# Performance work log

Hardware: AMD Instinct MI355X
Metric: run time of the kernel (lower is better)

The kernel has to match this reference:

```python
import jax, jax.numpy as jnp
import numpy as np

REG = 1.0
LAM1 = REG * 0.1
LAM2 = REG * 0.15
TAU = 0.01
RHO = 1.99
SIGMA = 1.0 / TAU / 72.0


def epsilon(I):
    # I: (c,h,w,2) -> G: (c,h,w,4); symmetrized gradient stencil
    I0, I1 = I[..., 0], I[..., 1]
    g0 = I0 - jnp.pad(I0[:, :-1, :], ((0, 0), (1, 0), (0, 0)))
    g1 = jnp.pad(I0[:, :, 1:] - I0[:, :, :-1], ((0, 0), (0, 0), (1, 0)))
    g2 = I1 - jnp.pad(I1[:, :, :-1], ((0, 0), (0, 0), (1, 0)))
    g3 = jnp.pad(I1[:, 1:, :] - I1[:, :-1, :], ((0, 0), (0, 1), (0, 0)))
    return jnp.stack([g0, g1, g2, g3], axis=-1)


def epsilonT(G):
    # G: (c,h,w,4) -> I: (c,h,w,2); adjoint of epsilon
    g0, g1, g2, g3 = G[..., 0], G[..., 1], G[..., 2], G[..., 3]
    i0 = g0 - jnp.pad(g0[:, 1:, :], ((0, 0), (0, 1), (0, 0)))
    A = g1[:, :, 1:]
    i0 = i0 + jnp.pad(A, ((0, 0), (0, 0), (1, 0))) - jnp.pad(A, ((0, 0), (0, 0), (0, 1)))
    i1 = g2 - jnp.pad(g2[:, :, 1:], ((0, 0), (0, 0), (0, 1)))
    B = g3[:, :-1, :]
    i1 = i1 + jnp.pad(B, ((0, 0), (1, 0), (0, 0))) - jnp.pad(B, ((0, 0), (0, 1), (0, 0)))
    return jnp.stack([i0, i1], axis=-1)


def nabla(I):
    # I: (c,h,w) -> G: (c,h,w,2); forward differences, zero at far boundary
    g0 = jnp.pad(I[:, 1:, :] - I[:, :-1, :], ((0, 0), (0, 1), (0, 0)))
    g1 = jnp.pad(I[:, :, 1:] - I[:, :, :-1], ((0, 0), (0, 0), (0, 1)))
    return jnp.stack([g0, g1], axis=-1)


def nablaT(G):
    # G: (c,h,w,2) -> I: (c,h,w); negative divergence (adjoint of nabla)
    A = G[:, :-1, :, 0]
    B = G[:, :, :-1, 1]
    return (jnp.pad(A, ((0, 0), (1, 0), (0, 0))) - jnp.pad(A, ((0, 0), (0, 1), (0, 0)))
            + jnp.pad(B, ((0, 0), (0, 0), (1, 0))) - jnp.pad(B, ((0, 0), (0, 0), (0, 1))))


def prox_tau_fx(x, y):
    return (x + TAU * y) / (1.0 + TAU)


def prox_tau_fr(r):
    left = jnp.sqrt(jnp.sum(r ** 2, axis=3)) / (TAU * LAM1)
    return r - r / jnp.maximum(left, 1.0)[..., None]


def prox_sigma_g_conj(u):
    return u / jnp.maximum(jnp.sqrt(jnp.sum(u ** 2, axis=3)) / LAM2, 1.0)[..., None]


def setup_inputs() -> dict:
    key = jax.random.key(0)
    y = jax.random.normal(key, (3, 512, 512), dtype=jnp.float32)
    return {"y": y, "n_it_max": 30}


def reference(y, n_it_max):
    c, h, w = y.shape
    x2 = y
    r2 = jnp.zeros((c, h, w, 2), dtype=y.dtype)
    u2 = jnp.zeros((c, h, w, 4), dtype=y.dtype)

    def step(carry, _):
        x2, r2, u2 = carry
        tmp = TAU * epsilonT(u2)
        x = prox_tau_fx(x2 - nablaT(tmp), y)
        r = prox_tau_fr(r2 + tmp)
        u = prox_sigma_g_conj(u2 + SIGMA * epsilon(nabla(2.0 * x - x2) - (2.0 * r - r2)))
        x2 = x2 + RHO * (x - x2)
        r2 = r2 + RHO * (r - r2)
        u2 = u2 + RHO * (u - u2)
        return (x2, r2, u2), None

    (x2, r2, u2), _ = jax.lax.scan(step, (x2, r2, u2), None, length=n_it_max)
    return (x2, r2, u2)
```

## Files before the change

kernel.cpp:

```cpp
#include <hip/hip_runtime.h>
#include <type_traits>


#define H 512
#define W 512
#define C 3
#define HW (H * W)
#define CHW (C * H * W)
#define N_IT 30

#define TW 64
#define TH 8

#define TAU     0.01f
#define LAM2    0.15f
#define RHO     1.99f
#define SIGMA   1.3888888888888888f
#define TL1     0.001f
#define INV_1PT (1.0f / 1.01f)

#define BROWS 10
#define BSTR  72

typedef _Float16 f16;
typedef __attribute__((ext_vector_type(4))) _Float16 h4;
typedef __attribute__((ext_vector_type(8))) _Float16 h8;


template <int MODE>
__global__ __launch_bounds__(192)
void fused_it(const float* __restrict__ y,
              const float* __restrict__ srcX,
              const f16*   __restrict__ srcH,
              float*       __restrict__ dstX,
              f16*         __restrict__ dstH,
              float*       __restrict__ outp)
{
    __shared__ float sb[3][BROWS][BSTR];

    const int tid = threadIdx.x;
    const int c   = blockIdx.z;
    const int i0  = blockIdx.y * TH;
    const int j0  = blockIdx.x * TW;
    const int cb  = c * HW;

    const bool edge = (MODE == 0) ||
                      (blockIdx.x == 0) || (blockIdx.x == W / TW - 1) ||
                      (blockIdx.y == 0) || (blockIdx.y == H / TH - 1);

    const f16* rSrc = srcH;
    const f16* uSrc = srcH + 2 * CHW;
    f16* rDst = dstH;
    f16* uDst = dstH ? dstH + 2 * CHW : nullptr;

    float cu0[4], cu1[4], cu2[4], cu3[4];

    auto strip1 = [&](auto SAFE_c, int rr, int s, bool interior) {
        constexpr bool SAFE = decltype(SAFE_c)::value;
        const int gi  = i0 + rr;
        const int gjb = j0 + s;
        const int p   = cb + gi * W + gjb;

        const bool rowC  = SAFE || ((unsigned)gi < H);
        const bool cMain = SAFE || ((unsigned)gjb < W);
        const bool okC   = rowC && cMain;

        float yv[4], x2c[4], r0c[4], r1c[4];
        if (okC) {
            *(float4*)yv = *(const float4*)(y + p);
        } else {
            yv[0] = yv[1] = yv[2] = yv[3] = 0.f;
        }
        if (MODE != 0) {
            if (okC) {
                *(float4*)x2c = *(const float4*)(srcX + p);
                const h8 rv = *(const h8*)(rSrc + 2 * p);
                #pragma unroll
                for (int e = 0; e < 4; ++e) {
                    r0c[e] = (float)rv[2 * e];
                    r1c[e] = (float)rv[2 * e + 1];
                }
            } else {
                #pragma unroll
                for (int e = 0; e < 4; ++e) { x2c[e] = 0.f; r0c[e] = 0.f; r1c[e] = 0.f; }
            }
        }

        float t0c[4], t1c[4], t0n[4], t1w[4];
        if (MODE == 0) {
            #pragma unroll
            for (int e = 0; e < 4; ++e) {
                x2c[e] = yv[e]; r0c[e] = 0.f; r1c[e] = 0.f;
                t0c[e] = t1c[e] = t0n[e] = t1w[e] = 0.f;
            }
            if (interior) {
                #pragma unroll
                for (int e = 0; e < 4; ++e) { cu0[e] = cu1[e] = cu2[e] = cu3[e] = 0.f; }
            }
        } else {
            const bool rowN = SAFE || ((unsigned)(gi - 1) < H);
            const bool rowS = SAFE || ((unsigned)(gi + 1) < H);
            const bool cm1  = SAFE || ((unsigned)(gjb - 1) < W);
            const bool c4   = SAFE || ((unsigned)(gjb + 4) < W);
            const int pN = p - W, pS = p + W;

            auto L4 = [&](int pp, bool ok) -> h4 {
                h4 z = {}; if (ok) z = *(const h4*)(uSrc + 4 * pp); return z;
            };
            auto L8 = [&](int pp, bool ok) -> h8 {
                h8 z = {}; if (ok) z = *(const h8*)(uSrc + 4 * pp); return z;
            };
            const h4 nA = L4(pN - 1, rowN && cm1);
            const h8 nB = L8(pN,     rowN && cMain);
            const h8 nC = L8(pN + 2, rowN && cMain);
            const h4 nD = L4(pN + 4, rowN && c4);
            const h4 cA = L4(p - 1,  rowC && cm1);
            const h8 cB = L8(p,      okC);
            const h8 cC = L8(p + 2,  okC);
            const h4 cD = L4(p + 4,  rowC && c4);
            const h8 sB = L8(pS,     rowS && cMain);
            const h8 sC = L8(pS + 2, rowS && cMain);

            const float u0c[4] = {(float)cB[0], (float)cB[4], (float)cC[0], (float)cC[4]};
            const float u1c[5] = {(float)cB[1], (float)cB[5], (float)cC[1], (float)cC[5], (float)cD[1]};
            const float u2r[6] = {(float)cA[2], (float)cB[2], (float)cB[6], (float)cC[2], (float)cC[6], (float)cD[2]};
            const float u3c[5] = {(float)cA[3], (float)cB[3], (float)cB[7], (float)cC[3], (float)cC[7]};
            const float u0n[4] = {(float)nB[0], (float)nB[4], (float)nC[0], (float)nC[4]};
            const float u1n[5] = {(float)nB[1], (float)nB[5], (float)nC[1], (float)nC[5], (float)nD[1]};
            const float u3n[5] = {(float)nA[3], (float)nB[3], (float)nB[7], (float)nC[3], (float)nC[7]};
            const float u0s[4] = {(float)sB[0], (float)sB[4], (float)sC[0], (float)sC[4]};

            if constexpr (SAFE) {
                #pragma unroll
                for (int e = 0; e < 4; ++e) {
                    t0c[e] = TAU * (u0c[e] - u0s[e] + u1c[e] - u1c[e + 1]);
                    t1c[e] = TAU * (u2r[e + 1] - u2r[e + 2] + u3n[e + 1] - u3c[e + 1]);
                    t0n[e] = TAU * (u0n[e] - u0c[e] + u1n[e] - u1n[e + 1]);
                    t1w[e] = TAU * (u2r[e] - u2r[e + 1] + u3n[e] - u3c[e]);
                }
            } else {
                const bool im0 = gi > 0, imHl = gi < H - 1;
                #pragma unroll
                for (int e = 0; e < 4; ++e) {
                    const int gj = gjb + e;
                    const bool jm0 = gj > 0;
                    t0c[e] = TAU * (u0c[e] - u0s[e] + (jm0 ? u1c[e] : 0.f) - u1c[e + 1]);
                    t1c[e] = TAU * (u2r[e + 1] - u2r[e + 2] + u3n[e + 1] - (imHl ? u3c[e + 1] : 0.f));
                    t0n[e] = im0 ? TAU * (u0n[e] - u0c[e] + (jm0 ? u1n[e] : 0.f) - u1n[e + 1]) : 0.f;
                    t1w[e] = jm0 ? TAU * (u2r[e] - u2r[e + 1] + u3n[e] - (imHl ? u3c[e] : 0.f)) : 0.f;
                }
            }
            if (interior) {
                #pragma unroll
                for (int e = 0; e < 4; ++e) {
                    cu0[e] = u0c[e]; cu1[e] = u1c[e];
                    cu2[e] = u2r[e + 1]; cu3[e] = u3c[e + 1];
                }
            }
        }

        float xnew[4], rn0[4], rn1[4], xb[4], rb0[4], rb1[4];
        {
            const bool imH = SAFE ? true : (gi < H - 1);
            #pragma unroll
            for (int e = 0; e < 4; ++e) {
                const int gj = gjb + e;
                const bool jmW = SAFE ? true : (gj < W - 1);
                const float nT  = t0n[e] - (imH ? t0c[e] : 0.f) + t1w[e] - (jmW ? t1c[e] : 0.f);
                const float xv  = (x2c[e] - nT + TAU * yv[e]) * INV_1PT;
                xb[e] = 2.f * xv - x2c[e];
                const float rp0 = r0c[e] + t0c[e];
                const float rp1 = r1c[e] + t1c[e];
                const float ss  = rp0 * rp0 + rp1 * rp1;
                const float f   = 1.f - fminf(TL1 * rsqrtf(ss), 1.f);
                const float rv0 = rp0 * f, rv1 = rp1 * f;
                rb0[e]  = 2.f * rv0 - r0c[e];
                rb1[e]  = 2.f * rv1 - r1c[e];
                xnew[e] = x2c[e] + RHO * (xv - x2c[e]);
                rn0[e]  = r0c[e] + RHO * (rv0 - r0c[e]);
                rn1[e]  = r1c[e] + RHO * (rv1 - r1c[e]);
            }
        }
        *(float4*)&sb[0][rr + 1][s + 4] = *(float4*)xb;
        *(float4*)&sb[1][rr + 1][s + 4] = *(float4*)rb0;
        *(float4*)&sb[2][rr + 1][s + 4] = *(float4*)rb1;

        if (interior) {
            if (MODE == 2) {
                *(float4*)(outp + p) = *(float4*)xnew;
                *(float4*)(outp + CHW + 2 * p)     = make_float4(rn0[0], rn1[0], rn0[1], rn1[1]);
                *(float4*)(outp + CHW + 2 * p + 4) = make_float4(rn0[2], rn1[2], rn0[3], rn1[3]);
            } else {
                *(float4*)(dstX + p) = *(float4*)xnew;
                h8 hr;
                #pragma unroll
                for (int e = 0; e < 4; ++e) {
                    hr[2 * e]     = (f16)rn0[e];
                    hr[2 * e + 1] = (f16)rn1[e];
                }
                *(h8*)(rDst + 2 * p) = hr;
            }
        }
    };

    auto ringmap = [&](int t, int& rr, int& s) {
        if (t < 18)      { rr = -1;      s = 4 * t - 4; }
        else if (t < 36) { rr = TH;      s = 4 * (t - 18) - 4; }
        else if (t < 44) { rr = t - 36;  s = -4; }
        else             { rr = t - 44;  s = TW; }
    };

    if (!edge) {
        if (tid < 128) {
            strip1(std::true_type{}, tid >> 4, 4 * (tid & 15), true);
        } else if (tid < 180) {
            int rr, s; ringmap(tid - 128, rr, s);
            strip1(std::true_type{}, rr, s, false);
        }
    } else {
        if (tid < 128) {
            strip1(std::false_type{}, tid >> 4, 4 * (tid & 15), true);
        } else if (tid < 180) {
            int rr, s; ringmap(tid - 128, rr, s);
            strip1(std::false_type{}, rr, s, false);
        }
    }
    __syncthreads();

    auto stage2 = [&](auto SAFE_c) {
        constexpr bool SAFE = decltype(SAFE_c)::value;
        const int tx = tid & 15, ty = tid >> 4;
        const int gi  = i0 + ty;
        const int gjb = j0 + 4 * tx;
        const int lr  = ty + 1;
        const int lc  = 4 * tx + 4;
        float4 v;
        float xA[6], xS[6], xN[4], r0C[5], r0N[4], r1C[5], r1S[4];
        xA[0] = sb[0][lr][lc - 1];
        v = *(const float4*)&sb[0][lr][lc]; xA[1]=v.x; xA[2]=v.y; xA[3]=v.z; xA[4]=v.w;
        xA[5] = sb[0][lr][lc + 4];
        xS[0] = sb[0][lr + 1][lc - 1];
        v = *(const float4*)&sb[0][lr + 1][lc]; xS[1]=v.x; xS[2]=v.y; xS[3]=v.z; xS[4]=v.w;
        xS[5] = sb[0][lr + 1][lc + 4];
        v = *(const float4*)&sb[0][lr - 1][lc]; xN[0]=v.x; xN[1]=v.y; xN[2]=v.z; xN[3]=v.w;
        r0C[0] = sb[1][lr][lc - 1];
        v = *(const float4*)&sb[1][lr][lc]; r0C[1]=v.x; r0C[2]=v.y; r0C[3]=v.z; r0C[4]=v.w;
        v = *(const float4*)&sb[1][lr - 1][lc]; r0N[0]=v.x; r0N[1]=v.y; r0N[2]=v.z; r0N[3]=v.w;
        r1C[0] = sb[2][lr][lc - 1];
        v = *(const float4*)&sb[2][lr][lc]; r1C[1]=v.x; r1C[2]=v.y; r1C[3]=v.z; r1C[4]=v.w;
        v = *(const float4*)&sb[2][lr + 1][lc]; r1S[0]=v.x; r1S[1]=v.y; r1S[2]=v.z; r1S[3]=v.w;

        const bool im0 = SAFE ? true : (gi > 0);
        const bool imH = SAFE ? true : (gi < H - 1);
        float un0[4], un1[4], un2[4], un3[4];
        #pragma unroll
        for (int e = 0; e < 4; ++e) {
            const int gj = gjb + e;
            const bool jm0 = SAFE ? true : (gj > 0);
            const bool jmW = SAFE ? true : (gj < W - 1);
            const float xC = xA[e + 1], xE = xA[e + 2], xW_ = xA[e];
            const float I0c = (imH ? xS[e + 1] - xC : 0.f) - r0C[e + 1];
            const float I0n = im0 ? (xC - xN[e] - r0N[e]) : 0.f;
            const float I0w = jm0 ? ((imH ? xS[e] - xW_ : 0.f) - r0C[e]) : 0.f;
            const float I1c = (jmW ? xE - xC : 0.f) - r1C[e + 1];
            const float I1w = jm0 ? (xC - xW_ - r1C[e]) : 0.f;
            const float I1s = imH ? ((jmW ? xS[e + 2] - xS[e + 1] : 0.f) - r1S[e]) : 0.f;
            const float g0 = I0c - I0n;
            const float g1 = jm0 ? (I0c - I0w) : 0.f;
            const float g2 = I1c - I1w;
            const float g3 = imH ? (I1s - I1c) : 0.f;
            const float up0 = cu0[e] + SIGMA * g0;
            const float up1 = cu1[e] + SIGMA * g1;
            const float up2 = cu2[e] + SIGMA * g2;
            const float up3 = cu3[e] + SIGMA * g3;
            const float ss  = up0 * up0 + up1 * up1 + up2 * up2 + up3 * up3;
            const float inv = fminf(LAM2 * rsqrtf(ss), 1.f);
            un0[e] = cu0[e] + RHO * (up0 * inv - cu0[e]);
            un1[e] = cu1[e] + RHO * (up1 * inv - cu1[e]);
            un2[e] = cu2[e] + RHO * (up2 * inv - cu2[e]);
            un3[e] = cu3[e] + RHO * (up3 * inv - cu3[e]);
        }
        const int p = cb + gi * W + gjb;
        if (MODE == 2) {
            #pragma unroll
            for (int e = 0; e < 4; ++e)
                *(float4*)(outp + 3 * CHW + 4 * (p + e)) =
                    make_float4(un0[e], un1[e], un2[e], un3[e]);
        } else {
            h8 w0, w1;
            #pragma unroll
            for (int e = 0; e < 2; ++e) {
                w0[4 * e + 0] = (f16)un0[e]; w0[4 * e + 1] = (f16)un1[e];
                w0[4 * e + 2] = (f16)un2[e]; w0[4 * e + 3] = (f16)un3[e];
            }
            #pragma unroll
            for (int e = 2; e < 4; ++e) {
                w1[4 * (e - 2) + 0] = (f16)un0[e]; w1[4 * (e - 2) + 1] = (f16)un1[e];
                w1[4 * (e - 2) + 2] = (f16)un2[e]; w1[4 * (e - 2) + 3] = (f16)un3[e];
            }
            *(h8*)(uDst + 4 * p)     = w0;
            *(h8*)(uDst + 4 * p + 8) = w1;
        }
    };

    if (tid < 128) {
        if (!edge) stage2(std::true_type{});
        else       stage2(std::false_type{});
    }
}

extern "C" void kernel_launch(void* const* d_in, const int* in_sizes, int n_in,
                              void* d_out, int out_size, void* d_ws, size_t ws_size,
                              hipStream_t stream) {
    const float* y = (const float*)d_in[0];
    float* out = (float*)d_out;

    float* x0 = (float*)d_ws;
    float* x1 = x0 + CHW;
    f16*   h0 = (f16*)(x1 + CHW);
    f16*   h1 = h0 + 6 * CHW;

    dim3 blk(192, 1, 1);
    dim3 grd(W / TW, H / TH, C);

    fused_it<0><<<grd, blk, 0, stream>>>(y, nullptr, nullptr, x0, h0, nullptr);
    for (int k = 2; k < N_IT; ++k) {
        const bool even = (k % 2 == 0);
        float* sx = even ? x0 : x1;  f16* sh = even ? h0 : h1;
        float* dx = even ? x1 : x0;  f16* dh = even ? h1 : h0;
        fused_it<1><<<grd, blk, 0, stream>>>(y, sx, sh, dx, dh, nullptr);
    }
    fused_it<2><<<grd, blk, 0, stream>>>(y, x0, h0, nullptr, nullptr, out);
}
```

Measured before the change: 335.2 us.

## Double tile height and process two rows per thread with shared vertical neighbors

Tile height doubles from 8 to 16 rows, and each of the 128 worker threads now computes two vertically adjacent rows in both stages. Loads of the u neighbor rows and shared-memory reads are reused between the two rows. This shrinks the redundant halo work and global loads per output. The cost is higher register pressure per thread and half as many blocks, which lowers parallelism.

```diff
diff --git a/kernel.cpp b/kernel.cpp
--- a/kernel.cpp
+++ b/kernel.cpp
@@ -10,7 +10,7 @@
 #define N_IT 30
 
 #define TW 64
-#define TH 8
+#define TH 16
 
 #define TAU     0.01f
 #define LAM2    0.15f
@@ -19,7 +19,7 @@
 #define TL1     0.001f
 #define INV_1PT (1.0f / 1.01f)
 
-#define BROWS 10
+#define BROWS 18
 #define BSTR  72
 
 typedef _Float16 f16;
@@ -53,16 +53,166 @@
     f16* rDst = dstH;
     f16* uDst = dstH ? dstH + 2 * CHW : nullptr;
 
-    float cu0[4], cu1[4], cu2[4], cu3[4];
-
-    auto strip1 = [&](auto SAFE_c, int rr, int s, bool interior) {
+    float cu0A[4], cu1A[4], cu2A[4], cu3A[4];
+    float cu0B[4], cu1B[4], cu2B[4], cu3B[4];
+
+    auto s1finish = [&](auto SAFE_c, int gi, int gjb, int p, int lrow, bool interior,
+                        const float* yv, const float* x2c, const float* r0c, const float* r1c,
+                        const float* t0c, const float* t1c, const float* t0n, const float* t1w) {
         constexpr bool SAFE = decltype(SAFE_c)::value;
+        const int s4 = gjb - j0 + 4;
+        const bool imH = SAFE ? true : (gi < H - 1);
+        float xb[4], rb0[4], rb1[4], xnew[4], rn0[4], rn1[4];
+        #pragma unroll
+        for (int e = 0; e < 4; ++e) {
+            const int gj = gjb + e;
+            const bool jmW = SAFE ? true : (gj < W - 1);
+            const float nT  = t0n[e] - (imH ? t0c[e] : 0.f) + t1w[e] - (jmW ? t1c[e] : 0.f);
+            const float xv  = (x2c[e] - nT + TAU * yv[e]) * INV_1PT;
+            xb[e] = 2.f * xv - x2c[e];
+            const float rp0 = r0c[e] + t0c[e];
+            const float rp1 = r1c[e] + t1c[e];
+            const float ss  = rp0 * rp0 + rp1 * rp1;
+            const float f   = 1.f - fminf(TL1 * rsqrtf(ss), 1.f);
+            const float rv0 = rp0 * f, rv1 = rp1 * f;
+            rb0[e]  = 2.f * rv0 - r0c[e];
+            rb1[e]  = 2.f * rv1 - r1c[e];
+            xnew[e] = x2c[e] + RHO * (xv - x2c[e]);
+            rn0[e]  = r0c[e] + RHO * (rv0 - r0c[e]);
+            rn1[e]  = r1c[e] + RHO * (rv1 - r1c[e]);
+        }
+        *(float4*)&sb[0][lrow][s4] = *(float4*)xb;
+        *(float4*)&sb[1][lrow][s4] = *(float4*)rb0;
+        *(float4*)&sb[2][lrow][s4] = *(float4*)rb1;
+
+        if (interior) {
+            if (MODE == 2) {
+                *(float4*)(outp + p) = *(float4*)xnew;
+                *(float4*)(outp + CHW + 2 * p)     = make_float4(rn0[0], rn1[0], rn0[1], rn1[1]);
+                *(float4*)(outp + CHW + 2 * p + 4) = make_float4(rn0[2], rn1[2], rn0[3], rn1[3]);
+            } else {
+                *(float4*)(dstX + p) = *(float4*)xnew;
+                h8 hr;
+                #pragma unroll
+                for (int e = 0; e < 4; ++e) {
+                    hr[2 * e]     = (f16)rn0[e];
+                    hr[2 * e + 1] = (f16)rn1[e];
+                }
+                *(h8*)(rDst + 2 * p) = hr;
+            }
+        }
+    };
+
+    auto tSafe = [&](const float* u0c, const float* u1c, const float* u2r, const float* u3c,
+                     const float* u0n, const float* u1n, const float* u3n, const float* u0s,
+                     float* t0c, float* t1c, float* t0n, float* t1w) {
+        #pragma unroll
+        for (int e = 0; e < 4; ++e) {
+            t0c[e] = TAU * (u0c[e] - u0s[e] + u1c[e] - u1c[e + 1]);
+            t1c[e] = TAU * (u2r[e + 1] - u2r[e + 2] + u3n[e + 1] - u3c[e + 1]);
+            t0n[e] = TAU * (u0n[e] - u0c[e] + u1n[e] - u1n[e + 1]);
+            t1w[e] = TAU * (u2r[e] - u2r[e + 1] + u3n[e] - u3c[e]);
+        }
+    };
+
+    auto U4 = [&](int pp) { return *(const h4*)(uSrc + 4 * pp); };
+    auto U8 = [&](int pp) { return *(const h8*)(uSrc + 4 * pp); };
+
+    auto pairSafe = [&](int r0, int s, bool interior) {
+        const int gi0 = i0 + r0, gjb = j0 + s;
+        const int p0 = cb + gi0 * W + gjb, pN = p0 - W, p1 = p0 + W, pS = p1 + W;
+
+        float yv0[4], yv1[4], x20[4], x21[4], r00[4], r01v[4], r10[4], r11v[4];
+        *(float4*)yv0 = *(const float4*)(y + p0);
+        *(float4*)yv1 = *(const float4*)(y + p1);
+        *(float4*)x20 = *(const float4*)(srcX + p0);
+        *(float4*)x21 = *(const float4*)(srcX + p1);
+        {
+            const h8 rv = *(const h8*)(rSrc + 2 * p0);
+            #pragma unroll
+            for (int e = 0; e < 4; ++e) { r00[e] = (float)rv[2 * e]; r10[e] = (float)rv[2 * e + 1]; }
+        }
+        {
+            const h8 rv = *(const h8*)(rSrc + 2 * p1);
+            #pragma unroll
+            for (int e = 0; e < 4; ++e) { r01v[e] = (float)rv[2 * e]; r11v[e] = (float)rv[2 * e + 1]; }
+        }
+        const h4 nA = U4(pN - 1); const h8 nB = U8(pN), nC = U8(pN + 2); const h4 nD = U4(pN + 4);
+        const h4 aA = U4(p0 - 1); const h8 aB = U8(p0), aC = U8(p0 + 2); const h4 aD = U4(p0 + 4);
+        const h4 bA = U4(p1 - 1); const h8 bB = U8(p1), bC = U8(p1 + 2); const h4 bD = U4(p1 + 4);
+        const h8 sB = U8(pS), sC = U8(pS + 2);
+
+        const float N0[4] = {(float)nB[0], (float)nB[4], (float)nC[0], (float)nC[4]};
+        const float N1[5] = {(float)nB[1], (float)nB[5], (float)nC[1], (float)nC[5], (float)nD[1]};
+        const float N3[5] = {(float)nA[3], (float)nB[3], (float)nB[7], (float)nC[3], (float)nC[7]};
+        const float A0[4] = {(float)aB[0], (float)aB[4], (float)aC[0], (float)aC[4]};
+        const float A1[5] = {(float)aB[1], (float)aB[5], (float)aC[1], (float)aC[5], (float)aD[1]};
+        const float A2[6] = {(float)aA[2], (float)aB[2], (float)aB[6], (float)aC[2], (float)aC[6], (float)aD[2]};
+        const float A3[5] = {(float)aA[3], (float)aB[3], (float)aB[7], (float)aC[3], (float)aC[7]};
+        const float B0[4] = {(float)bB[0], (float)bB[4], (float)bC[0], (float)bC[4]};
+        const float B1[5] = {(float)bB[1], (float)bB[5], (float)bC[1], (float)bC[5], (float)bD[1]};
+        const float B2[6] = {(float)bA[2], (float)bB[2], (float)bB[6], (float)bC[2], (float)bC[6], (float)bD[2]};
+        const float B3[5] = {(float)bA[3], (float)bB[3], (float)bB[7], (float)bC[3], (float)bC[7]};
+        const float S0[4] = {(float)sB[0], (float)sB[4], (float)sC[0], (float)sC[4]};
+
+        float t0c[4], t1c[4], t0n[4], t1w[4];
+        tSafe(A0, A1, A2, A3, N0, N1, N3, B0, t0c, t1c, t0n, t1w);
+        if (interior) {
+            #pragma unroll
+            for (int e = 0; e < 4; ++e) {
+                cu0A[e] = A0[e]; cu1A[e] = A1[e]; cu2A[e] = A2[e + 1]; cu3A[e] = A3[e + 1];
+            }
+        }
+        s1finish(std::true_type{}, gi0, gjb, p0, r0 + 1, interior, yv0, x20, r00, r10,
+                 t0c, t1c, t0n, t1w);
+        tSafe(B0, B1, B2, B3, A0, A1, A3, S0, t0c, t1c, t0n, t1w);
+        if (interior) {
+            #pragma unroll
+            for (int e = 0; e < 4; ++e) {
+                cu0B[e] = B0[e]; cu1B[e] = B1[e]; cu2B[e] = B2[e + 1]; cu3B[e] = B3[e + 1];
+            }
+        }
+        s1finish(std::true_type{}, gi0 + 1, gjb, p1, r0 + 2, interior, yv1, x21, r01v, r11v,
+                 t0c, t1c, t0n, t1w);
+    };
+
+    auto singleSafe = [&](int rr, int s) {
+        const int gi = i0 + rr, gjb = j0 + s;
+        const int p = cb + gi * W + gjb, pN = p - W, pS = p + W;
+        float yv[4], x2c[4], r0c[4], r1c[4];
+        *(float4*)yv  = *(const float4*)(y + p);
+        *(float4*)x2c = *(const float4*)(srcX + p);
+        {
+            const h8 rv = *(const h8*)(rSrc + 2 * p);
+            #pragma unroll
+            for (int e = 0; e < 4; ++e) { r0c[e] = (float)rv[2 * e]; r1c[e] = (float)rv[2 * e + 1]; }
+        }
+        const h4 nA = U4(pN - 1); const h8 nB = U8(pN), nC = U8(pN + 2); const h4 nD = U4(pN + 4);
+        const h4 cA = U4(p - 1);  const h8 cB = U8(p),  cC = U8(p + 2);  const h4 cD = U4(p + 4);
+        const h8 sB = U8(pS), sC = U8(pS + 2);
+
+        const float u0c[4] = {(float)cB[0], (float)cB[4], (float)cC[0], (float)cC[4]};
+        const float u1c[5] = {(float)cB[1], (float)cB[5], (float)cC[1], (float)cC[5], (float)cD[1]};
+        const float u2r[6] = {(float)cA[2], (float)cB[2], (float)cB[6], (float)cC[2], (float)cC[6], (float)cD[2]};
+        const float u3c[5] = {(float)cA[3], (float)cB[3], (float)cB[7], (float)cC[3], (float)cC[7]};
+        const float u0n[4] = {(float)nB[0], (float)nB[4], (float)nC[0], (float)nC[4]};
+        const float u1n[5] = {(float)nB[1], (float)nB[5], (float)nC[1], (float)nC[5], (float)nD[1]};
+        const float u3n[5] = {(float)nA[3], (float)nB[3], (float)nB[7], (float)nC[3], (float)nC[7]};
+        const float u0s[4] = {(float)sB[0], (float)sB[4], (float)sC[0], (float)sC[4]};
+
+        float t0c[4], t1c[4], t0n[4], t1w[4];
+        tSafe(u0c, u1c, u2r, u3c, u0n, u1n, u3n, u0s, t0c, t1c, t0n, t1w);
+        s1finish(std::true_type{}, gi, gjb, p, rr + 1, false, yv, x2c, r0c, r1c,
+                 t0c, t1c, t0n, t1w);
+    };
+
+    auto edgeRow = [&](int rr, int s, bool interior,
+                       float* cu0s, float* cu1s, float* cu2s, float* cu3s) {
         const int gi  = i0 + rr;
         const int gjb = j0 + s;
         const int p   = cb + gi * W + gjb;
-
-        const bool rowC  = SAFE || ((unsigned)gi < H);
-        const bool cMain = SAFE || ((unsigned)gjb < W);
+        const bool rowC  = (unsigned)gi < H;
+        const bool cMain = (unsigned)gjb < W;
         const bool okC   = rowC && cMain;
 
         float yv[4], x2c[4], r0c[4], r1c[4];
@@ -76,10 +226,7 @@
                 *(float4*)x2c = *(const float4*)(srcX + p);
                 const h8 rv = *(const h8*)(rSrc + 2 * p);
                 #pragma unroll
-                for (int e = 0; e < 4; ++e) {
-                    r0c[e] = (float)rv[2 * e];
-                    r1c[e] = (float)rv[2 * e + 1];
-                }
+                for (int e = 0; e < 4; ++e) { r0c[e] = (float)rv[2 * e]; r1c[e] = (float)rv[2 * e + 1]; }
             } else {
                 #pragma unroll
                 for (int e = 0; e < 4; ++e) { x2c[e] = 0.f; r0c[e] = 0.f; r1c[e] = 0.f; }
@@ -95,13 +242,13 @@
             }
             if (interior) {
                 #pragma unroll
-                for (int e = 0; e < 4; ++e) { cu0[e] = cu1[e] = cu2[e] = cu3[e] = 0.f; }
+                for (int e = 0; e < 4; ++e) { cu0s[e] = cu1s[e] = cu2s[e] = cu3s[e] = 0.f; }
             }
         } else {
-            const bool rowN = SAFE || ((unsigned)(gi - 1) < H);
-            const bool rowS = SAFE || ((unsigned)(gi + 1) < H);
-            const bool cm1  = SAFE || ((unsigned)(gjb - 1) < W);
-            const bool c4   = SAFE || ((unsigned)(gjb + 4) < W);
+            const bool rowN = (unsigned)(gi - 1) < H;
+            const bool rowS = (unsigned)(gi + 1) < H;
+            const bool cm1  = (unsigned)(gjb - 1) < W;
+            const bool c4   = (unsigned)(gjb + 4) < W;
             const int pN = p - W, pS = p + W;
 
             auto L4 = [&](int pp, bool ok) -> h4 {
@@ -130,126 +277,63 @@
             const float u3n[5] = {(float)nA[3], (float)nB[3], (float)nB[7], (float)nC[3], (float)nC[7]};
             const float u0s[4] = {(float)sB[0], (float)sB[4], (float)sC[0], (float)sC[4]};
 
-            if constexpr (SAFE) {
-                #pragma unroll
-                for (int e = 0; e < 4; ++e) {
-                    t0c[e] = TAU * (u0c[e] - u0s[e] + u1c[e] - u1c[e + 1]);
-                    t1c[e] = TAU * (u2r[e + 1] - u2r[e + 2] + u3n[e + 1] - u3c[e + 1]);
-                    t0n[e] = TAU * (u0n[e] - u0c[e] + u1n[e] - u1n[e + 1]);
-                    t1w[e] = TAU * (u2r[e] - u2r[e + 1] + u3n[e] - u3c[e]);
-                }
-            } else {
-                const bool im0 = gi > 0, imHl = gi < H - 1;
-                #pragma unroll
-                for (int e = 0; e < 4; ++e) {
-                    const int gj = gjb + e;
-                    const bool jm0 = gj > 0;
-                    t0c[e] = TAU * (u0c[e] - u0s[e] + (jm0 ? u1c[e] : 0.f) - u1c[e + 1]);
-                    t1c[e] = TAU * (u2r[e + 1] - u2r[e + 2] + u3n[e + 1] - (imHl ? u3c[e + 1] : 0.f));
-                    t0n[e] = im0 ? TAU * (u0n[e] - u0c[e] + (jm0 ? u1n[e] : 0.f) - u1n[e + 1]) : 0.f;
-                    t1w[e] = jm0 ? TAU * (u2r[e] - u2r[e + 1] + u3n[e] - (imHl ? u3c[e] : 0.f)) : 0.f;
-                }
+            const bool im0 = gi > 0, imHl = gi < H - 1;
+            #pragma unroll
+            for (int e = 0; e < 4; ++e) {
+                const int gj = gjb + e;
+                const bool jm0 = gj > 0;
+                t0c[e] = TAU * (u0c[e] - u0s[e] + (jm0 ? u1c[e] : 0.f) - u1c[e + 1]);
+                t1c[e] = TAU * (u2r[e + 1] - u2r[e + 2] + u3n[e + 1] - (imHl ? u3c[e + 1] : 0.f));
+                t0n[e] = im0 ? TAU * (u0n[e] - u0c[e] + (jm0 ? u1n[e] : 0.f) - u1n[e + 1]) : 0.f;
+                t1w[e] = jm0 ? TAU * (u2r[e] - u2r[e + 1] + u3n[e] - (imHl ? u3c[e] : 0.f)) : 0.f;
             }
             if (interior) {
                 #pragma unroll
                 for (int e = 0; e < 4; ++e) {
-                    cu0[e] = u0c[e]; cu1[e] = u1c[e];
-                    cu2[e] = u2r[e + 1]; cu3[e] = u3c[e + 1];
+                    cu0s[e] = u0c[e]; cu1s[e] = u1c[e];
+                    cu2s[e] = u2r[e + 1]; cu3s[e] = u3c[e + 1];
                 }
             }
         }
-
-        float xnew[4], rn0[4], rn1[4], xb[4], rb0[4], rb1[4];
-        {
-            const bool imH = SAFE ? true : (gi < H - 1);
-            #pragma unroll
-            for (int e = 0; e < 4; ++e) {
-                const int gj = gjb + e;
-                const bool jmW = SAFE ? true : (gj < W - 1);
-                const float nT  = t0n[e] - (imH ? t0c[e] : 0.f) + t1w[e] - (jmW ? t1c[e] : 0.f);
-                const float xv  = (x2c[e] - nT + TAU * yv[e]) * INV_1PT;
-                xb[e] = 2.f * xv - x2c[e];
-                const float rp0 = r0c[e] + t0c[e];
-                const float rp1 = r1c[e] + t1c[e];
-                const float ss  = rp0 * rp0 + rp1 * rp1;
-                const float f   = 1.f - fminf(TL1 * rsqrtf(ss), 1.f);
-                const float rv0 = rp0 * f, rv1 = rp1 * f;
-                rb0[e]  = 2.f * rv0 - r0c[e];
-                rb1[e]  = 2.f * rv1 - r1c[e];
-                xnew[e] = x2c[e] + RHO * (xv - x2c[e]);
-                rn0[e]  = r0c[e] + RHO * (rv0 - r0c[e]);
-                rn1[e]  = r1c[e] + RHO * (rv1 - r1c[e]);
-            }
-        }
-        *(float4*)&sb[0][rr + 1][s + 4] = *(float4*)xb;
-        *(float4*)&sb[1][rr + 1][s + 4] = *(float4*)rb0;
-        *(float4*)&sb[2][rr + 1][s + 4] = *(float4*)rb1;
-
-        if (interior) {
-            if (MODE == 2) {
-                *(float4*)(outp + p) = *(float4*)xnew;
-                *(float4*)(outp + CHW + 2 * p)     = make_float4(rn0[0], rn1[0], rn0[1], rn1[1]);
-                *(float4*)(outp + CHW + 2 * p + 4) = make_float4(rn0[2], rn1[2], rn0[3], rn1[3]);
-            } else {
-                *(float4*)(dstX + p) = *(float4*)xnew;
-                h8 hr;
-                #pragma unroll
-                for (int e = 0; e < 4; ++e) {
-                    hr[2 * e]     = (f16)rn0[e];
-                    hr[2 * e + 1] = (f16)rn1[e];
-                }
-                *(h8*)(rDst + 2 * p) = hr;
-            }
-        }
-    };
-
-    auto ringmap = [&](int t, int& rr, int& s) {
-        if (t < 18)      { rr = -1;      s = 4 * t - 4; }
-        else if (t < 36) { rr = TH;      s = 4 * (t - 18) - 4; }
-        else if (t < 44) { rr = t - 36;  s = -4; }
-        else             { rr = t - 44;  s = TW; }
+        s1finish(std::false_type{}, gi, gjb, p, rr + 1, interior, yv, x2c, r0c, r1c,
+                 t0c, t1c, t0n, t1w);
     };
 
     if (!edge) {
         if (tid < 128) {
-            strip1(std::true_type{}, tid >> 4, 4 * (tid & 15), true);
+            pairSafe(2 * (tid >> 4), 4 * (tid & 15), true);
         } else if (tid < 180) {
-            int rr, s; ringmap(tid - 128, rr, s);
-            strip1(std::true_type{}, rr, s, false);
+            const int t = tid - 128;
+            if (t < 18)      singleSafe(-1, 4 * t - 4);
+            else if (t < 36) singleSafe(TH, 4 * (t - 18) - 4);
+            else if (t < 44) pairSafe(2 * (t - 36), -4, false);
+            else             pairSafe(2 * (t - 44), TW, false);
         }
     } else {
         if (tid < 128) {
-            strip1(std::false_type{}, tid >> 4, 4 * (tid & 15), true);
+            const int r0v = 2 * (tid >> 4), sv = 4 * (tid & 15);
+            edgeRow(r0v,     sv, true, cu0A, cu1A, cu2A, cu3A);
+            edgeRow(r0v + 1, sv, true, cu0B, cu1B, cu2B, cu3B);
         } else if (tid < 180) {
-            int rr, s; ringmap(tid - 128, rr, s);
-            strip1(std::false_type{}, rr, s, false);
+            const int t = tid - 128;
+            if (t < 18)      edgeRow(-1, 4 * t - 4, false, cu0A, cu1A, cu2A, cu3A);
+            else if (t < 36) edgeRow(TH, 4 * (t - 18) - 4, false, cu0A, cu1A, cu2A, cu3A);
+            else if (t < 44) {
+                edgeRow(2 * (t - 36),     -4, false, cu0A, cu1A, cu2A, cu3A);
+                edgeRow(2 * (t - 36) + 1, -4, false, cu0A, cu1A, cu2A, cu3A);
+            } else {
+                edgeRow(2 * (t - 44),     TW, false, cu0A, cu1A, cu2A, cu3A);
+                edgeRow(2 * (t - 44) + 1, TW, false, cu0A, cu1A, cu2A, cu3A);
+            }
         }
     }
     __syncthreads();
 
-    auto stage2 = [&](auto SAFE_c) {
+    auto s2row = [&](auto SAFE_c, int gi, int gjb, int p,
+                     const float* xA, const float* xS, const float* xN,
+                     const float* r0C, const float* r0N, const float* r1C, const float* r1S,
+                     const float* cu0s, const float* cu1s, const float* cu2s, const float* cu3s) {
         constexpr bool SAFE = decltype(SAFE_c)::value;
-        const int tx = tid & 15, ty = tid >> 4;
-        const int gi  = i0 + ty;
-        const int gjb = j0 + 4 * tx;
-        const int lr  = ty + 1;
-        const int lc  = 4 * tx + 4;
-        float4 v;
-        float xA[6], xS[6], xN[4], r0C[5], r0N[4], r1C[5], r1S[4];
-        xA[0] = sb[0][lr][lc - 1];
-        v = *(const float4*)&sb[0][lr][lc]; xA[1]=v.x; xA[2]=v.y; xA[3]=v.z; xA[4]=v.w;
-        xA[5] = sb[0][lr][lc + 4];
-        xS[0] = sb[0][lr + 1][lc - 1];
-        v = *(const float4*)&sb[0][lr + 1][lc]; xS[1]=v.x; xS[2]=v.y; xS[3]=v.z; xS[4]=v.w;
-        xS[5] = sb[0][lr + 1][lc + 4];
-        v = *(const float4*)&sb[0][lr - 1][lc]; xN[0]=v.x; xN[1]=v.y; xN[2]=v.z; xN[3]=v.w;
-        r0C[0] = sb[1][lr][lc - 1];
-        v = *(const float4*)&sb[1][lr][lc]; r0C[1]=v.x; r0C[2]=v.y; r0C[3]=v.z; r0C[4]=v.w;
-        v = *(const float4*)&sb[1][lr - 1][lc]; r0N[0]=v.x; r0N[1]=v.y; r0N[2]=v.z; r0N[3]=v.w;
-        r1C[0] = sb[2][lr][lc - 1];
-        v = *(const float4*)&sb[2][lr][lc]; r1C[1]=v.x; r1C[2]=v.y; r1C[3]=v.z; r1C[4]=v.w;
-        v = *(const float4*)&sb[2][lr + 1][lc]; r1S[0]=v.x; r1S[1]=v.y; r1S[2]=v.z; r1S[3]=v.w;
-
         const bool im0 = SAFE ? true : (gi > 0);
         const bool imH = SAFE ? true : (gi < H - 1);
         float un0[4], un1[4], un2[4], un3[4];
@@ -269,18 +353,17 @@
             const float g1 = jm0 ? (I0c - I0w) : 0.f;
             const float g2 = I1c - I1w;
             const float g3 = imH ? (I1s - I1c) : 0.f;
-            const float up0 = cu0[e] + SIGMA * g0;
-            const float up1 = cu1[e] + SIGMA * g1;
-            const float up2 = cu2[e] + SIGMA * g2;
-            const float up3 = cu3[e] + SIGMA * g3;
+            const float up0 = cu0s[e] + SIGMA * g0;
+            const float up1 = cu1s[e] + SIGMA * g1;
+            const float up2 = cu2s[e] + SIGMA * g2;
+            const float up3 = cu3s[e] + SIGMA * g3;
             const float ss  = up0 * up0 + up1 * up1 + up2 * up2 + up3 * up3;
             const float inv = fminf(LAM2 * rsqrtf(ss), 1.f);
-            un0[e] = cu0[e] + RHO * (up0 * inv - cu0[e]);
-            un1[e] = cu1[e] + RHO * (up1 * inv - cu1[e]);
-            un2[e] = cu2[e] + RHO * (up2 * inv - cu2[e]);
-            un3[e] = cu3[e] + RHO * (up3 * inv - cu3[e]);
-        }
-        const int p = cb + gi * W + gjb;
+            un0[e] = cu0s[e] + RHO * (up0 * inv - cu0s[e]);
+            un1[e] = cu1s[e] + RHO * (up1 * inv - cu1s[e]);
+            un2[e] = cu2s[e] + RHO * (up2 * inv - cu2s[e]);
+            un3[e] = cu3s[e] + RHO * (up3 * inv - cu3s[e]);
+        }
         if (MODE == 2) {
             #pragma unroll
             for (int e = 0; e < 4; ++e)
@@ -304,8 +387,84 @@
     };
 
     if (tid < 128) {
-        if (!edge) stage2(std::true_type{});
-        else       stage2(std::false_type{});
+        const int tx = tid & 15, q = tid >> 4;
+        const int r0 = 2 * q;
+        const int gi0 = i0 + r0, gjb = j0 + 4 * tx;
+        const int p0 = cb + gi0 * W + gjb;
+        const int lr0 = r0 + 1, lr1 = r0 + 2, lc = 4 * tx + 4;
+
+        if (!edge) {
+            float4 v;
+            float xNr[4];
+            v = *(const float4*)&sb[0][lr0 - 1][lc]; xNr[0]=v.x; xNr[1]=v.y; xNr[2]=v.z; xNr[3]=v.w;
+            float xAr[6];
+            xAr[0] = sb[0][lr0][lc - 1];
+            v = *(const float4*)&sb[0][lr0][lc]; xAr[1]=v.x; xAr[2]=v.y; xAr[3]=v.z; xAr[4]=v.w;
+            xAr[5] = sb[0][lr0][lc + 4];
+            float xMr[6];
+            xMr[0] = sb[0][lr1][lc - 1];
+            v = *(const float4*)&sb[0][lr1][lc]; xMr[1]=v.x; xMr[2]=v.y; xMr[3]=v.z; xMr[4]=v.w;
+            xMr[5] = sb[0][lr1][lc + 4];
+            float xSr[6];
+            xSr[0] = sb[0][lr1 + 1][lc - 1];
+            v = *(const float4*)&sb[0][lr1 + 1][lc]; xSr[1]=v.x; xSr[2]=v.y; xSr[3]=v.z; xSr[4]=v.w;
+            xSr[5] = sb[0][lr1 + 1][lc + 4];
+            float r0Nr[4];
+            v = *(const float4*)&sb[1][lr0 - 1][lc]; r0Nr[0]=v.x; r0Nr[1]=v.y; r0Nr[2]=v.z; r0Nr[3]=v.w;
+            float r0Ca[5];
+            r0Ca[0] = sb[1][lr0][lc - 1];
+            v = *(const float4*)&sb[1][lr0][lc]; r0Ca[1]=v.x; r0Ca[2]=v.y; r0Ca[3]=v.z; r0Ca[4]=v.w;
+            float r0Cb[5];
+            r0Cb[0] = sb[1][lr1][lc - 1];
+            v = *(const float4*)&sb[1][lr1][lc]; r0Cb[1]=v.x; r0Cb[2]=v.y; r0Cb[3]=v.z; r0Cb[4]=v.w;
+            float r1Ca[5];
+            r1Ca[0] = sb[2][lr0][lc - 1];
+            v = *(const float4*)&sb[2][lr0][lc]; r1Ca[1]=v.x; r1Ca[2]=v.y; r1Ca[3]=v.z; r1Ca[4]=v.w;
+            float r1Cb[5];
+            r1Cb[0] = sb[2][lr1][lc - 1];
+            v = *(const float4*)&sb[2][lr1][lc]; r1Cb[1]=v.x; r1Cb[2]=v.y; r1Cb[3]=v.z; r1Cb[4]=v.w;
+            float r1Sr[4];
+            v = *(const float4*)&sb[2][lr1 + 1][lc]; r1Sr[0]=v.x; r1Sr[1]=v.y; r1Sr[2]=v.z; r1Sr[3]=v.w;
+
+            const float r1S0[4] = {r1Cb[1], r1Cb[2], r1Cb[3], r1Cb[4]};
+            s2row(std::true_type{}, gi0, gjb, p0,
+                  xAr, xMr, xNr, r0Ca, r0Nr, r1Ca, r1S0,
+                  cu0A, cu1A, cu2A, cu3A);
+            const float xN1[4]  = {xAr[1], xAr[2], xAr[3], xAr[4]};
+            const float r0N1[4] = {r0Ca[1], r0Ca[2], r0Ca[3], r0Ca[4]};
+            s2row(std::true_type{}, gi0 + 1, gjb, p0 + W,
+                  xMr, xSr, xN1, r0Cb, r0N1, r1Cb, r1Sr,
+                  cu0B, cu1B, cu2B, cu3B);
+        } else {
+            #pragma unroll
+            for (int slot = 0; slot < 2; ++slot) {
+                const int rr = r0 + slot;
+                const int gi = i0 + rr;
+                const int lr = rr + 1;
+                const int p  = cb + gi * W + gjb;
+                float4 v;
+                float xA[6], xS[6], xN[4], r0C[5], r0N[4], r1C[5], r1S[4];
+                xA[0] = sb[0][lr][lc - 1];
+                v = *(const float4*)&sb[0][lr][lc]; xA[1]=v.x; xA[2]=v.y; xA[3]=v.z; xA[4]=v.w;
+                xA[5] = sb[0][lr][lc + 4];
+                xS[0] = sb[0][lr + 1][lc - 1];
+                v = *(const float4*)&sb[0][lr + 1][lc]; xS[1]=v.x; xS[2]=v.y; xS[3]=v.z; xS[4]=v.w;
+                xS[5] = sb[0][lr + 1][lc + 4];
+                v = *(const float4*)&sb[0][lr - 1][lc]; xN[0]=v.x; xN[1]=v.y; xN[2]=v.z; xN[3]=v.w;
+                r0C[0] = sb[1][lr][lc - 1];
+                v = *(const float4*)&sb[1][lr][lc]; r0C[1]=v.x; r0C[2]=v.y; r0C[3]=v.z; r0C[4]=v.w;
+                v = *(const float4*)&sb[1][lr - 1][lc]; r0N[0]=v.x; r0N[1]=v.y; r0N[2]=v.z; r0N[3]=v.w;
+                r1C[0] = sb[2][lr][lc - 1];
+                v = *(const float4*)&sb[2][lr][lc]; r1C[1]=v.x; r1C[2]=v.y; r1C[3]=v.z; r1C[4]=v.w;
+                v = *(const float4*)&sb[2][lr + 1][lc]; r1S[0]=v.x; r1S[1]=v.y; r1S[2]=v.z; r1S[3]=v.w;
+                if (slot == 0)
+                    s2row(std::false_type{}, gi, gjb, p, xA, xS, xN, r0C, r0N, r1C, r1S,
+                          cu0A, cu1A, cu2A, cu3A);
+                else
+                    s2row(std::false_type{}, gi, gjb, p, xA, xS, xN, r0C, r0N, r1C, r1S,
+                          cu0B, cu1B, cu2B, cu3B);
+            }
+        }
     }
 }
 
```

Result: slower. 547.4 us (+63.3%).
